# Optimization experiments

Hardware: AMD Instinct MI355X
Metric: run time of the kernel (lower is better)

The kernel has to match this reference:

```python
import jax, jax.numpy as jnp
import numpy as np

N, F, BS, EMB, C = 768, 16, 2, 32, 2
GAMMA, EXT_COEFF = 0.9, 1.0
HU = 2 * EMB          # util FF hidden = emb_dim*2
HE = 2 * (EMB + C)    # ext FF hidden = (emb_dim+output_channel)*2
HV = 2 * EMB          # val FF hidden = emb_dim*2


def setup_inputs() -> dict:
    key = jax.random.key(0)
    ks = jax.random.split(key, 16)
    s = 0.1
    p = lambda k, shape: jax.random.normal(k, shape, dtype=jnp.float32) * s
    x = jax.random.normal(ks[0], (1, N, F), dtype=jnp.float32)
    pi = jax.random.uniform(ks[1], (BS, N, N, C), dtype=jnp.float32)
    # sparse-ish dense adjacency (avg degree ~ 0.03*N), self loops so softmax rows are valid
    adj = (jax.random.uniform(ks[2], (N, N)) < 0.03).astype(jnp.float32)
    adj = jnp.maximum(adj, jnp.eye(N, dtype=jnp.float32))
    return {
        "x": x, "bs": BS, "pi": pi, "i": 0, "adj": adj,
        # GAT (global / local), single head, depth 1: proj W, attention vectors a_src/a_dst
        "Wg": p(ks[3], (F, EMB)), "asg": p(ks[4], (EMB,)), "adg": p(ks[5], (EMB,)),
        "Wl": p(ks[6], (F, EMB)), "asl": p(ks[7], (EMB,)), "adl": p(ks[8], (EMB,)),
        # util FF: 2*emb -> HU -> 1, output act = -softplus
        "uW1": p(ks[9], (2 * EMB, HU)), "ub1": jnp.zeros((HU,), jnp.float32),
        "uW2": p(ks[10], (HU, 1)), "ub2": jnp.zeros((1,), jnp.float32),
        # ext FF: 2*emb + C -> HE -> 1
        "eW1": p(ks[11], (2 * EMB + C, HE)), "eb1": jnp.zeros((HE,), jnp.float32),
        "eW2": p(ks[12], (HE, 1)), "eb2": jnp.zeros((1,), jnp.float32),
        # val FF: emb -> HV -> 1
        "vW1": p(ks[13], (EMB, HV)), "vb1": jnp.zeros((HV,), jnp.float32),
        "vW2": p(ks[14], (HV, 1)), "vb2": jnp.zeros((1,), jnp.float32),
    }


def _gat(xr, adj, W, a_src, a_dst):
    # single-head GAT layer masked by dense adjacency
    h = xr @ W                                                  # [bs, n, e]
    e = (h @ a_src)[:, :, None] + (h @ a_dst)[:, None, :]      # [bs, n, n]
    e = jax.nn.leaky_relu(e, 0.2)
    e = jnp.where(adj[None] > 0, e, -1e9)
    att = jax.nn.softmax(e, axis=-1)
    return att @ h                                              # [bs, n, e]


def reference(x, bs, pi, i, adj, Wg, asg, adg, Wl, asl, adl,
              uW1, ub1, uW2, ub2, eW1, eb1, eW2, eb2, vW1, vb1, vW2, vb2):
    n = x.shape[1]
    xr = jnp.broadcast_to(x, (bs, n, x.shape[2]))
    # global GAT -> value head
    yg = _gat(xr, adj, Wg, asg, adg)                            # [bs, n, e]
    val = -jax.nn.softplus(jax.nn.relu(yg @ vW1 + vb1) @ vW2 + vb2)[..., 0]  # [bs, n]
    # util: FF on z[b,i,j] = concat(yg_i, yg_j); fuse by splitting the first layer
    ur = yg @ uW1[:EMB]                                         # row half  [bs, n, HU]
    uc = yg @ uW1[EMB:]                                         # col half  [bs, n, HU]
    uh = jax.nn.relu(ur[:, :, None, :] + uc[:, None, :, :] + ub1)  # [bs, n, n, HU]
    util = -jax.nn.softplus((uh @ uW2)[..., 0] + ub2[0]) * adj[None]
    # ext: local GAT, z concat with pi along feature dim, same split trick
    yl = _gat(xr, adj, Wl, asl, adl)
    er = yl @ eW1[:EMB]
    ec = yl @ eW1[EMB:2 * EMB]
    ep = pi @ eW1[2 * EMB:]                                     # [bs, n, n, HE]
    eh = jax.nn.relu(er[:, :, None, :] + ec[:, None, :, :] + ep + eb1)
    ext = -jax.nn.softplus((eh @ eW2)[..., 0] + eb2[0]) * adj[None]
    f_val = util + EXT_COEFF * ext + GAMMA * val[:, None, :] - val[:, :, None]
    return f_val
```

## Files before the change

kernel.cpp:

```cpp
#include <hip/hip_runtime.h>
#include <math.h>

#define NN 768
#define FD 16
#define EMB 32
#define HU 64
#define HE 68
#define GAMMA 0.9f

__device__ __forceinline__ float softplus_f(float x) {
    return fmaxf(x, 0.f) + log1pf(__expf(-fabsf(x)));
}

__global__ __launch_bounds__(256) void k_gatheads(
    const float* __restrict__ x, const float* __restrict__ adj,
    const float* __restrict__ Wg, const float* __restrict__ asg, const float* __restrict__ adg,
    const float* __restrict__ Wl, const float* __restrict__ asl, const float* __restrict__ adl,
    const float* __restrict__ uW1, const float* __restrict__ ub1,
    const float* __restrict__ eW1, const float* __restrict__ eb1,
    const float* __restrict__ vW1, const float* __restrict__ vb1,
    const float* __restrict__ vW2, const float* __restrict__ vb2,
    float* __restrict__ urb, float* __restrict__ ucR,
    float* __restrict__ erb, float* __restrict__ ecR,
    float* __restrict__ val, int* __restrict__ nbrg, int* __restrict__ cntg)
{
    int b = blockIdx.x;
    int i = b >> 1, which = b & 1;
    int t = threadIdx.x;
    int lane = t & 63, wid = t >> 6;
    int gid = t >> 5, l32 = t & 31;

    __shared__ float sW[FD * EMB];
    __shared__ float sas[EMB], sad[EMB];
    __shared__ int   s_nbr[NN];
    __shared__ int   s_wcnt[4];
    __shared__ float s_acc[8][EMB + 1];
    __shared__ float s_sum[8];
    __shared__ float s_y[EMB];

    {
        const float* Wsrc = which ? Wl : Wg;
        const float* assrc = which ? asl : asg;
        const float* adsrc = which ? adl : adg;
        for (int k = t; k < FD * EMB; k += 256) sW[k] = Wsrc[k];
        if (t < EMB) { sas[t] = assrc[t]; sad[t] = adsrc[t]; }
    }

    const float* arow = adj + (size_t)i * NN;

    unsigned long long masks[3];
    int wbase = wid * 192;
    int mycnt = 0;
#pragma unroll
    for (int s = 0; s < 3; ++s) {
        int j = wbase + s * 64 + lane;
        bool act = arow[j] > 0.f;
        masks[s] = __ballot(act);
        mycnt += (int)__popcll(masks[s]);
    }
    if (lane == 0) s_wcnt[wid] = mycnt;
    __syncthreads();
    int run = 0;
    for (int w = 0; w < wid; ++w) run += s_wcnt[w];
#pragma unroll
    for (int s = 0; s < 3; ++s) {
        bool act = (masks[s] >> lane) & 1ULL;
        int pos = run + (int)__popcll(masks[s] & ((1ULL << lane) - 1ULL));
        if (act) s_nbr[pos] = wbase + s * 64 + lane;
        run += (int)__popcll(masks[s]);
    }
    __syncthreads();
    int M = s_wcnt[0] + s_wcnt[1] + s_wcnt[2] + s_wcnt[3];

    float si;
    {
        const float4* x4 = (const float4*)(x + i * FD);
        float4 xa = x4[0], xb = x4[1], xc = x4[2], xd = x4[3];
        float xv[FD] = {xa.x, xa.y, xa.z, xa.w, xb.x, xb.y, xb.z, xb.w,
                        xc.x, xc.y, xc.z, xc.w, xd.x, xd.y, xd.z, xd.w};
        float he = 0.f;
#pragma unroll
        for (int f = 0; f < FD; ++f) he += xv[f] * sW[f * EMB + l32];
        float d = he * sas[l32];
#pragma unroll
        for (int off = 16; off >= 1; off >>= 1) d += __shfl_xor(d, off);
        si = d;
    }

    float acc = 0.f, psum = 0.f;
    for (int c0 = 0; c0 < M; c0 += 8) {
        int idx = c0 + gid;
        if (idx < M) {
            int jn = s_nbr[idx];
            const float4* x4 = (const float4*)(x + jn * FD);
            float4 xa = x4[0], xb = x4[1], xc = x4[2], xd = x4[3];
            float xv[FD] = {xa.x, xa.y, xa.z, xa.w, xb.x, xb.y, xb.z, xb.w,
                            xc.x, xc.y, xc.z, xc.w, xd.x, xd.y, xd.z, xd.w};
            float h = 0.f;
#pragma unroll
            for (int f = 0; f < FD; ++f) h += xv[f] * sW[f * EMB + l32];
            float d = h * sad[l32];
#pragma unroll
            for (int off = 16; off >= 1; off >>= 1) d += __shfl_xor(d, off);
            float e = si + d;
            e = (e > 0.f) ? e : 0.2f * e;
            float p = __expf(e);
            acc += p * h;
            psum += p;
        }
    }
    s_acc[gid][l32] = acc;
    if (l32 == 0) s_sum[gid] = psum;
    __syncthreads();
    if (t < EMB) {
        float s = 0.f, sp = 0.f;
#pragma unroll
        for (int g = 0; g < 8; ++g) { s += s_acc[g][t]; sp += s_sum[g]; }
        s_y[t] = s / sp;
    }
    __syncthreads();

    if (which == 0) {
        if (t < HU) {
            float r = ub1[t], cc = 0.f;
#pragma unroll
            for (int e = 0; e < EMB; ++e) {
                float y = s_y[e];
                r  += y * uW1[e * HU + t];
                cc += y * uW1[(e + EMB) * HU + t];
            }
            urb[i * HU + t] = r;
            ucR[i * HU + t] = cc;
        } else if (t >= 192) {
            int u = t - 192;
            float v = vb1[u];
#pragma unroll
            for (int e = 0; e < EMB; ++e) v += s_y[e] * vW1[e * 64 + u];
            float rv = fmaxf(v, 0.f) * vW2[u];
#pragma unroll
            for (int off = 32; off >= 1; off >>= 1) rv += __shfl_xor(rv, off);
            if (u == 0) val[i] = -softplus_f(rv + vb2[0]);
        }
        for (int idx = t; idx < M; idx += 256) nbrg[(size_t)i * NN + idx] = s_nbr[idx];
        if (t == 0) cntg[i] = M;
    } else {
        if (t < HE) {
            float r = eb1[t], cc = 0.f;
#pragma unroll
            for (int e = 0; e < EMB; ++e) {
                float y = s_y[e];
                r  += y * eW1[e * HE + t];
                cc += y * eW1[(e + EMB) * HE + t];
            }
            erb[i * HE + t] = r;
            ecR[i * HE + t] = cc;
        }
    }
}

__global__ __launch_bounds__(256) void k_final(
    const float* __restrict__ pi,
    const float* __restrict__ urb, const float* __restrict__ ucR,
    const float* __restrict__ erb, const float* __restrict__ ecR,
    const float* __restrict__ val,
    const float* __restrict__ uW2, const float* __restrict__ ub2,
    const float* __restrict__ eW1, const float* __restrict__ eb2,
    const float* __restrict__ eW2,
    const int* __restrict__ nbrg, const int* __restrict__ cntg,
    float* __restrict__ out)
{
    int i = blockIdx.x;
    int t = threadIdx.x;
    int lane = t & 63, wid = t >> 6;
    __shared__ float ur_s[HU], uW2s[HU], er_s[HE], eW2s[HE], w0[HE], w1[HE];
    if (t < HU) { ur_s[t] = urb[i * HU + t]; uW2s[t] = uW2[t]; }
    if (t < HE) {
        er_s[t] = erb[i * HE + t];
        eW2s[t] = eW2[t];
        w0[t] = eW1[(2 * EMB) * HE + t];
        w1[t] = eW1[(2 * EMB + 1) * HE + t];
    }
    __syncthreads();

    float vi = val[i];
    if (t < NN / 4) {
        float4 vv = ((const float4*)val)[t];
        float4 b;
        b.x = GAMMA * vv.x - vi;
        b.y = GAMMA * vv.y - vi;
        b.z = GAMMA * vv.z - vi;
        b.w = GAMMA * vv.w - vi;
        ((float4*)(out + (size_t)i * NN))[t] = b;
        ((float4*)(out + (size_t)(NN + i) * NN))[t] = b;
    }
    __syncthreads();

    int M = cntg[i];
    float ub2v = ub2[0], eb2v = eb2[0];

    int es = wid * 8 + (lane >> 3);
    int sub = lane & 7;

    for (int idx = es; idx < M; idx += 32) {
        int jn = nbrg[(size_t)i * NN + idx];
        const float4* uc4 = (const float4*)(ucR + (size_t)jn * HU);
        float accu = 0.f;
        {
            float4 u0 = uc4[sub * 2], u1 = uc4[sub * 2 + 1];
            int h = sub * 8;
            accu += fmaxf(ur_s[h + 0] + u0.x, 0.f) * uW2s[h + 0];
            accu += fmaxf(ur_s[h + 1] + u0.y, 0.f) * uW2s[h + 1];
            accu += fmaxf(ur_s[h + 2] + u0.z, 0.f) * uW2s[h + 2];
            accu += fmaxf(ur_s[h + 3] + u0.w, 0.f) * uW2s[h + 3];
            accu += fmaxf(ur_s[h + 4] + u1.x, 0.f) * uW2s[h + 4];
            accu += fmaxf(ur_s[h + 5] + u1.y, 0.f) * uW2s[h + 5];
            accu += fmaxf(ur_s[h + 6] + u1.z, 0.f) * uW2s[h + 6];
            accu += fmaxf(ur_s[h + 7] + u1.w, 0.f) * uW2s[h + 7];
        }
        float2 p0 = *(const float2*)(pi + ((size_t)i * NN + jn) * 2);
        float2 p1 = *(const float2*)(pi + ((size_t)(NN + i) * NN + jn) * 2);
        const float4* ec4 = (const float4*)(ecR + (size_t)jn * HE);
        float a0 = 0.f, a1 = 0.f;
        {
            float4 e0 = ec4[sub * 2], e1 = ec4[sub * 2 + 1];
            int h = sub * 8;
            float c;
            c = er_s[h + 0] + e0.x;
            a0 += fmaxf(c + p0.x * w0[h + 0] + p0.y * w1[h + 0], 0.f) * eW2s[h + 0];
            a1 += fmaxf(c + p1.x * w0[h + 0] + p1.y * w1[h + 0], 0.f) * eW2s[h + 0];
            c = er_s[h + 1] + e0.y;
            a0 += fmaxf(c + p0.x * w0[h + 1] + p0.y * w1[h + 1], 0.f) * eW2s[h + 1];
            a1 += fmaxf(c + p1.x * w0[h + 1] + p1.y * w1[h + 1], 0.f) * eW2s[h + 1];
            c = er_s[h + 2] + e0.z;
            a0 += fmaxf(c + p0.x * w0[h + 2] + p0.y * w1[h + 2], 0.f) * eW2s[h + 2];
            a1 += fmaxf(c + p1.x * w0[h + 2] + p1.y * w1[h + 2], 0.f) * eW2s[h + 2];
            c = er_s[h + 3] + e0.w;
            a0 += fmaxf(c + p0.x * w0[h + 3] + p0.y * w1[h + 3], 0.f) * eW2s[h + 3];
            a1 += fmaxf(c + p1.x * w0[h + 3] + p1.y * w1[h + 3], 0.f) * eW2s[h + 3];
            c = er_s[h + 4] + e1.x;
            a0 += fmaxf(c + p0.x * w0[h + 4] + p0.y * w1[h + 4], 0.f) * eW2s[h + 4];
            a1 += fmaxf(c + p1.x * w0[h + 4] + p1.y * w1[h + 4], 0.f) * eW2s[h + 4];
            c = er_s[h + 5] + e1.y;
            a0 += fmaxf(c + p0.x * w0[h + 5] + p0.y * w1[h + 5], 0.f) * eW2s[h + 5];
            a1 += fmaxf(c + p1.x * w0[h + 5] + p1.y * w1[h + 5], 0.f) * eW2s[h + 5];
            c = er_s[h + 6] + e1.z;
            a0 += fmaxf(c + p0.x * w0[h + 6] + p0.y * w1[h + 6], 0.f) * eW2s[h + 6];
            a1 += fmaxf(c + p1.x * w0[h + 6] + p1.y * w1[h + 6], 0.f) * eW2s[h + 6];
            c = er_s[h + 7] + e1.w;
            a0 += fmaxf(c + p0.x * w0[h + 7] + p0.y * w1[h + 7], 0.f) * eW2s[h + 7];
            a1 += fmaxf(c + p1.x * w0[h + 7] + p1.y * w1[h + 7], 0.f) * eW2s[h + 7];
            if (sub < 4) {
                int h2 = 64 + sub;
                float ce = er_s[h2] + ecR[(size_t)jn * HE + h2];
                a0 += fmaxf(ce + p0.x * w0[h2] + p0.y * w1[h2], 0.f) * eW2s[h2];
                a1 += fmaxf(ce + p1.x * w0[h2] + p1.y * w1[h2], 0.f) * eW2s[h2];
            }
        }
#pragma unroll
        for (int off = 4; off >= 1; off >>= 1) {
            accu += __shfl_xor(accu, off);
            a0   += __shfl_xor(a0, off);
            a1   += __shfl_xor(a1, off);
        }
        if (sub == 0) {
            float util = -softplus_f(accu + ub2v);
            float ext0 = -softplus_f(a0 + eb2v);
            float ext1 = -softplus_f(a1 + eb2v);
            float basej = GAMMA * val[jn] - vi;
            out[(size_t)i * NN + jn]        = basej + util + ext0;
            out[(size_t)(NN + i) * NN + jn] = basej + util + ext1;
        }
    }
}

extern "C" void kernel_launch(void* const* d_in, const int* in_sizes, int n_in,
                              void* d_out, int out_size, void* d_ws, size_t ws_size,
                              hipStream_t stream) {
    const float* x   = (const float*)d_in[0];
    const float* pi  = (const float*)d_in[2];
    const float* adj = (const float*)d_in[4];
    const float* Wg  = (const float*)d_in[5];
    const float* asg = (const float*)d_in[6];
    const float* adg = (const float*)d_in[7];
    const float* Wl  = (const float*)d_in[8];
    const float* asl = (const float*)d_in[9];
    const float* adl = (const float*)d_in[10];
    const float* uW1 = (const float*)d_in[11];
    const float* ub1 = (const float*)d_in[12];
    const float* uW2 = (const float*)d_in[13];
    const float* ub2 = (const float*)d_in[14];
    const float* eW1 = (const float*)d_in[15];
    const float* eb1 = (const float*)d_in[16];
    const float* eW2 = (const float*)d_in[17];
    const float* eb2 = (const float*)d_in[18];
    const float* vW1 = (const float*)d_in[19];
    const float* vb1 = (const float*)d_in[20];
    const float* vW2 = (const float*)d_in[21];
    const float* vb2 = (const float*)d_in[22];
    float* out = (float*)d_out;

    float* ws = (float*)d_ws;
    float* valp = ws;  ws += NN;
    float* urb  = ws;  ws += NN * HU;
    float* ucR  = ws;  ws += NN * HU;
    float* erb  = ws;  ws += NN * HE;
    float* ecR  = ws;  ws += NN * HE;
    int*   nbrg = (int*)ws;
    int*   cntg = nbrg + (size_t)NN * NN;

    k_gatheads<<<2 * NN, 256, 0, stream>>>(x, adj, Wg, asg, adg, Wl, asl, adl,
                                           uW1, ub1, eW1, eb1, vW1, vb1, vW2, vb2,
                                           urb, ucR, erb, ecR, valp, nbrg, cntg);
    k_final<<<NN, 256, 0, stream>>>(pi, urb, ucR, erb, ecR, valp,
                                    uW2, ub2, eW1, eb2, eW2, nbrg, cntg, out);
}
```

Measured before the change: 20.88 us.

## Split final kernel across batch and keep per-row weights in registers

The final kernel now launches one block per (row, batch) pair instead of one per row, so each block computes a single ext output and writes one output row. Per-row FF parameters (ur, er, uW2, eW2, pi weights) are loaded straight into registers as float4 instead of staged through shared memory. This removes a shared-memory staging phase and barrier and doubles the block count to improve occupancy for a lightly loaded, latency-bound kernel. In exchange, the util MLP and neighbor-list reads are repeated once per batch.

```diff
diff --git a/kernel.cpp b/kernel.cpp
--- a/kernel.cpp
+++ b/kernel.cpp
@@ -169,20 +169,38 @@
     const int* __restrict__ nbrg, const int* __restrict__ cntg,
     float* __restrict__ out)
 {
-    int i = blockIdx.x;
+    int bb = blockIdx.x;
+    int i = bb >> 1, bt = bb & 1;
     int t = threadIdx.x;
-    int lane = t & 63, wid = t >> 6;
-    __shared__ float ur_s[HU], uW2s[HU], er_s[HE], eW2s[HE], w0[HE], w1[HE];
-    if (t < HU) { ur_s[t] = urb[i * HU + t]; uW2s[t] = uW2[t]; }
-    if (t < HE) {
-        er_s[t] = erb[i * HE + t];
-        eW2s[t] = eW2[t];
-        w0[t] = eW1[(2 * EMB) * HE + t];
-        w1[t] = eW1[(2 * EMB + 1) * HE + t];
-    }
-    __syncthreads();
-
+    int es = t >> 3;
+    int sub = t & 7;
+    int h0 = sub * 8;
+
+    float4 urA = *(const float4*)(urb + i * HU + h0);
+    float4 urB = *(const float4*)(urb + i * HU + h0 + 4);
+    float4 uwA = *(const float4*)(uW2 + h0);
+    float4 uwB = *(const float4*)(uW2 + h0 + 4);
+    float4 erA = *(const float4*)(erb + i * HE + h0);
+    float4 erB = *(const float4*)(erb + i * HE + h0 + 4);
+    float4 ewA = *(const float4*)(eW2 + h0);
+    float4 ewB = *(const float4*)(eW2 + h0 + 4);
+    float4 w0A = *(const float4*)(eW1 + (2 * EMB) * HE + h0);
+    float4 w0B = *(const float4*)(eW1 + (2 * EMB) * HE + h0 + 4);
+    float4 w1A = *(const float4*)(eW1 + (2 * EMB + 1) * HE + h0);
+    float4 w1B = *(const float4*)(eW1 + (2 * EMB + 1) * HE + h0 + 4);
+    int h2 = 64 + sub;
+    float er_t = 0.f, ew_t = 0.f, w0_t = 0.f, w1_t = 0.f;
+    if (sub < 4) {
+        er_t = erb[i * HE + h2];
+        ew_t = eW2[h2];
+        w0_t = eW1[(2 * EMB) * HE + h2];
+        w1_t = eW1[(2 * EMB + 1) * HE + h2];
+    }
     float vi = val[i];
+    float ub2v = ub2[0], eb2v = eb2[0];
+
+    float* orow = out + ((size_t)bt * NN + i) * NN;
+
     if (t < NN / 4) {
         float4 vv = ((const float4*)val)[t];
         float4 b;
@@ -190,85 +208,49 @@
         b.y = GAMMA * vv.y - vi;
         b.z = GAMMA * vv.z - vi;
         b.w = GAMMA * vv.w - vi;
-        ((float4*)(out + (size_t)i * NN))[t] = b;
-        ((float4*)(out + (size_t)(NN + i) * NN))[t] = b;
+        ((float4*)orow)[t] = b;
     }
     __syncthreads();
 
     int M = cntg[i];
-    float ub2v = ub2[0], eb2v = eb2[0];
-
-    int es = wid * 8 + (lane >> 3);
-    int sub = lane & 7;
-
     for (int idx = es; idx < M; idx += 32) {
         int jn = nbrg[(size_t)i * NN + idx];
         const float4* uc4 = (const float4*)(ucR + (size_t)jn * HU);
+        float4 u0 = uc4[sub * 2], u1 = uc4[sub * 2 + 1];
         float accu = 0.f;
-        {
-            float4 u0 = uc4[sub * 2], u1 = uc4[sub * 2 + 1];
-            int h = sub * 8;
-            accu += fmaxf(ur_s[h + 0] + u0.x, 0.f) * uW2s[h + 0];
-            accu += fmaxf(ur_s[h + 1] + u0.y, 0.f) * uW2s[h + 1];
-            accu += fmaxf(ur_s[h + 2] + u0.z, 0.f) * uW2s[h + 2];
-            accu += fmaxf(ur_s[h + 3] + u0.w, 0.f) * uW2s[h + 3];
-            accu += fmaxf(ur_s[h + 4] + u1.x, 0.f) * uW2s[h + 4];
-            accu += fmaxf(ur_s[h + 5] + u1.y, 0.f) * uW2s[h + 5];
-            accu += fmaxf(ur_s[h + 6] + u1.z, 0.f) * uW2s[h + 6];
-            accu += fmaxf(ur_s[h + 7] + u1.w, 0.f) * uW2s[h + 7];
-        }
-        float2 p0 = *(const float2*)(pi + ((size_t)i * NN + jn) * 2);
-        float2 p1 = *(const float2*)(pi + ((size_t)(NN + i) * NN + jn) * 2);
+        accu += fmaxf(urA.x + u0.x, 0.f) * uwA.x;
+        accu += fmaxf(urA.y + u0.y, 0.f) * uwA.y;
+        accu += fmaxf(urA.z + u0.z, 0.f) * uwA.z;
+        accu += fmaxf(urA.w + u0.w, 0.f) * uwA.w;
+        accu += fmaxf(urB.x + u1.x, 0.f) * uwB.x;
+        accu += fmaxf(urB.y + u1.y, 0.f) * uwB.y;
+        accu += fmaxf(urB.z + u1.z, 0.f) * uwB.z;
+        accu += fmaxf(urB.w + u1.w, 0.f) * uwB.w;
+        float2 p = *(const float2*)(pi + (((size_t)bt * NN + i) * NN + jn) * 2);
         const float4* ec4 = (const float4*)(ecR + (size_t)jn * HE);
-        float a0 = 0.f, a1 = 0.f;
-        {
-            float4 e0 = ec4[sub * 2], e1 = ec4[sub * 2 + 1];
-            int h = sub * 8;
-            float c;
-            c = er_s[h + 0] + e0.x;
-            a0 += fmaxf(c + p0.x * w0[h + 0] + p0.y * w1[h + 0], 0.f) * eW2s[h + 0];
-            a1 += fmaxf(c + p1.x * w0[h + 0] + p1.y * w1[h + 0], 0.f) * eW2s[h + 0];
-            c = er_s[h + 1] + e0.y;
-            a0 += fmaxf(c + p0.x * w0[h + 1] + p0.y * w1[h + 1], 0.f) * eW2s[h + 1];
-            a1 += fmaxf(c + p1.x * w0[h + 1] + p1.y * w1[h + 1], 0.f) * eW2s[h + 1];
-            c = er_s[h + 2] + e0.z;
-            a0 += fmaxf(c + p0.x * w0[h + 2] + p0.y * w1[h + 2], 0.f) * eW2s[h + 2];
-            a1 += fmaxf(c + p1.x * w0[h + 2] + p1.y * w1[h + 2], 0.f) * eW2s[h + 2];
-            c = er_s[h + 3] + e0.w;
-            a0 += fmaxf(c + p0.x * w0[h + 3] + p0.y * w1[h + 3], 0.f) * eW2s[h + 3];
-            a1 += fmaxf(c + p1.x * w0[h + 3] + p1.y * w1[h + 3], 0.f) * eW2s[h + 3];
-            c = er_s[h + 4] + e1.x;
-            a0 += fmaxf(c + p0.x * w0[h + 4] + p0.y * w1[h + 4], 0.f) * eW2s[h + 4];
-            a1 += fmaxf(c + p1.x * w0[h + 4] + p1.y * w1[h + 4], 0.f) * eW2s[h + 4];
-            c = er_s[h + 5] + e1.y;
-            a0 += fmaxf(c + p0.x * w0[h + 5] + p0.y * w1[h + 5], 0.f) * eW2s[h + 5];
-            a1 += fmaxf(c + p1.x * w0[h + 5] + p1.y * w1[h + 5], 0.f) * eW2s[h + 5];
-            c = er_s[h + 6] + e1.z;
-            a0 += fmaxf(c + p0.x * w0[h + 6] + p0.y * w1[h + 6], 0.f) * eW2s[h + 6];
-            a1 += fmaxf(c + p1.x * w0[h + 6] + p1.y * w1[h + 6], 0.f) * eW2s[h + 6];
-            c = er_s[h + 7] + e1.w;
-            a0 += fmaxf(c + p0.x * w0[h + 7] + p0.y * w1[h + 7], 0.f) * eW2s[h + 7];
-            a1 += fmaxf(c + p1.x * w0[h + 7] + p1.y * w1[h + 7], 0.f) * eW2s[h + 7];
-            if (sub < 4) {
-                int h2 = 64 + sub;
-                float ce = er_s[h2] + ecR[(size_t)jn * HE + h2];
-                a0 += fmaxf(ce + p0.x * w0[h2] + p0.y * w1[h2], 0.f) * eW2s[h2];
-                a1 += fmaxf(ce + p1.x * w0[h2] + p1.y * w1[h2], 0.f) * eW2s[h2];
-            }
+        float4 e0 = ec4[sub * 2], e1 = ec4[sub * 2 + 1];
+        float a0 = 0.f;
+        a0 += fmaxf(erA.x + e0.x + p.x * w0A.x + p.y * w1A.x, 0.f) * ewA.x;
+        a0 += fmaxf(erA.y + e0.y + p.x * w0A.y + p.y * w1A.y, 0.f) * ewA.y;
+        a0 += fmaxf(erA.z + e0.z + p.x * w0A.z + p.y * w1A.z, 0.f) * ewA.z;
+        a0 += fmaxf(erA.w + e0.w + p.x * w0A.w + p.y * w1A.w, 0.f) * ewA.w;
+        a0 += fmaxf(erB.x + e1.x + p.x * w0B.x + p.y * w1B.x, 0.f) * ewB.x;
+        a0 += fmaxf(erB.y + e1.y + p.x * w0B.y + p.y * w1B.y, 0.f) * ewB.y;
+        a0 += fmaxf(erB.z + e1.z + p.x * w0B.z + p.y * w1B.z, 0.f) * ewB.z;
+        a0 += fmaxf(erB.w + e1.w + p.x * w0B.w + p.y * w1B.w, 0.f) * ewB.w;
+        if (sub < 4) {
+            float ce = er_t + ecR[(size_t)jn * HE + h2];
+            a0 += fmaxf(ce + p.x * w0_t + p.y * w1_t, 0.f) * ew_t;
         }
 #pragma unroll
         for (int off = 4; off >= 1; off >>= 1) {
             accu += __shfl_xor(accu, off);
             a0   += __shfl_xor(a0, off);
-            a1   += __shfl_xor(a1, off);
         }
         if (sub == 0) {
             float util = -softplus_f(accu + ub2v);
-            float ext0 = -softplus_f(a0 + eb2v);
-            float ext1 = -softplus_f(a1 + eb2v);
-            float basej = GAMMA * val[jn] - vi;
-            out[(size_t)i * NN + jn]        = basej + util + ext0;
-            out[(size_t)(NN + i) * NN + jn] = basej + util + ext1;
+            float ext  = -softplus_f(a0 + eb2v);
+            orow[jn] = GAMMA * val[jn] - vi + util + ext;
         }
     }
 }
@@ -311,6 +293,6 @@
     k_gatheads<<<2 * NN, 256, 0, stream>>>(x, adj, Wg, asg, adg, Wl, asl, adl,
                                            uW1, ub1, eW1, eb1, vW1, vb1, vW2, vb2,
                                            urb, ucR, erb, ecR, valp, nbrg, cntg);
-    k_final<<<NN, 256, 0, stream>>>(pi, urb, ucR, erb, ecR, valp,
-                                    uW2, ub2, eW1, eb2, eW2, nbrg, cntg, out);
-}
+    k_final<<<2 * NN, 256, 0, stream>>>(pi, urb, ucR, erb, ecR, valp,
+                                        uW2, ub2, eW1, eb2, eW2, nbrg, cntg, out);
+}
```

Measured after the change: 22.27 us. 1.07x slower.
